# Kernel tuning notes

Hardware: AMD Instinct MI355X
Metric: run time of the kernel (lower is better)

The kernel has to match this reference:

```python
import jax, jax.numpy as jnp
import numpy as np

B, S, E, H = 2, 2048, 1024, 16
Dh = E // H
LN_EPS = 1e-5


def setup_inputs() -> dict:
    key = jax.random.key(0)
    ks = jax.random.split(key, 12)
    std = 1.0 / np.sqrt(E)
    inp = {
        "query": jax.random.normal(ks[0], (B, S, E), jnp.float32),
        "key":   jax.random.normal(ks[1], (B, S, E), jnp.float32),
        "value": jax.random.normal(ks[2], (B, S, E), jnp.float32),
        # True = masked. Causal mask so every row keeps >=1 valid entry.
        "mask": jnp.broadcast_to(jnp.triu(jnp.ones((S, S), bool), k=1), (B, S, S)),
        # per-head QKV projections, stacked: weight [H, Dh, E] (torch Linear layout), bias [H, Dh]
        "Wq_w": jax.random.uniform(ks[3], (H, Dh, E), jnp.float32, -std, std),
        "Wq_b": jax.random.uniform(ks[4], (H, Dh), jnp.float32, -std, std),
        "Wk_w": jax.random.uniform(ks[5], (H, Dh, E), jnp.float32, -std, std),
        "Wk_b": jax.random.uniform(ks[6], (H, Dh), jnp.float32, -std, std),
        "Wv_w": jax.random.uniform(ks[7], (H, Dh, E), jnp.float32, -std, std),
        "Wv_b": jax.random.uniform(ks[8], (H, Dh), jnp.float32, -std, std),
        # output projection [E, E] (torch layout: out = x @ W.T + b)
        "out_w": jax.random.uniform(ks[9], (E, E), jnp.float32, -std, std),
        "out_b": jax.random.uniform(ks[10], (E,), jnp.float32, -std, std),
        "ln_g": jnp.ones((E,), jnp.float32),
        "ln_b": jnp.zeros((E,), jnp.float32),
    }
    return inp


def reference(query, key, value, mask, Wq_w, Wq_b, Wk_w, Wk_b, Wv_w, Wv_b, out_w, out_b, ln_g, ln_b):
    # per-head projections (batched over heads): [B,S,E] x [H,Dh,E] -> [B,H,S,Dh]
    q = jnp.einsum('bse,hde->bhsd', query, Wq_w) + Wq_b[None, :, None, :]
    k = jnp.einsum('bse,hde->bhsd', key,   Wk_w) + Wk_b[None, :, None, :]
    v = jnp.einsum('bse,hde->bhsd', value, Wv_w) + Wv_b[None, :, None, :]
    scale = 1.0 / np.sqrt(Dh).astype(np.float32)
    scores = jnp.einsum('bhsd,bhtd->bhst', q, k) * scale  # [B,H,S,S]
    scores = jnp.where(mask[:, None, :, :], -jnp.inf, scores)
    probs = jax.nn.softmax(scores, axis=-1)  # dropout p=0 (eval)
    ctx = jnp.einsum('bhst,bhtd->bhsd', probs, v)  # [B,H,S,Dh]
    att = ctx.transpose(0, 2, 1, 3).reshape(query.shape[0], query.shape[1], -1)  # concat heads [B,S,E]
    proj = att @ out_w.T + out_b  # dropout p=0
    x = query + proj  # residual
    mu = jnp.mean(x, axis=-1, keepdims=True)
    var = jnp.mean(jnp.square(x - mu), axis=-1, keepdims=True)
    return (x - mu) * jax.lax.rsqrt(var + LN_EPS) * ln_g + ln_b
```

## Files before the change

kernel.cpp:

```cpp
#include <hip/hip_runtime.h>
#include <stdint.h>

#define B_ 2
#define S_ 2048
#define E_ 1024
#define H_ 16
#define DH 64
#define M_TOT (B_*S_)

typedef short s16x8 __attribute__((ext_vector_type(8)));
typedef float f32x4 __attribute__((ext_vector_type(4)));
typedef unsigned int u32;
typedef unsigned short u16;

union V8 { uint4 u; s16x8 v; };

__device__ __forceinline__ u32 fbits(float f){ union{float f;u32 i;}x; x.f=f; return x.i; }
__device__ __forceinline__ u32 prround(float f){ return fbits(f)+0x8000u; }
__device__ __forceinline__ u16 f2bf(float f){ return (u16)(prround(f)>>16); }
__device__ __forceinline__ u32 permpack(u32 hi,u32 lo){ return __builtin_amdgcn_perm(hi,lo,0x07060302u); }
__device__ __forceinline__ uint4 pack8r(const float4 a, const float4 b){
    uint4 p;
    p.x = permpack(prround(a.y),prround(a.x));
    p.y = permpack(prround(a.w),prround(a.z));
    p.z = permpack(prround(b.y),prround(b.x));
    p.w = permpack(prround(b.w),prround(b.z));
    return p;
}
__device__ __forceinline__ float exp2_fast(float x){ float r; asm("v_exp_f32 %0, %1":"=v"(r):"v"(x)); return r; }

typedef const __attribute__((address_space(1))) u32* gas_t;
typedef __attribute__((address_space(3))) u32* las_t;
#define GLDS16(gp, lp) __builtin_amdgcn_global_load_lds((gas_t)(gp), (las_t)(lp), 16, 0, 0)

__global__ __launch_bounds__(256) void cvtw(
    const float* __restrict__ w0, const float* __restrict__ w1, const float* __restrict__ w2,
    u16* __restrict__ dst, int n4)
{
    const int z = blockIdx.y;
    const float* s = (z==0)?w0:(z==1)?w1:w2;
    u16* d = dst + (size_t)z*E_*E_;
    int i = blockIdx.x*256 + threadIdx.x;
    const int stride = gridDim.x*256;
    for (; i<n4; i+=stride){
        float4 v = ((const float4*)s)[i];
        uint2 p;
        p.x = permpack(prround(v.y),prround(v.x));
        p.y = permpack(prround(v.w),prround(v.z));
        ((uint2*)d)[i] = p;
    }
}
__global__ __launch_bounds__(256) void cvt1(
    const float* __restrict__ s, u16* __restrict__ d, int n4)
{
    int i = blockIdx.x*256 + threadIdx.x;
    const int stride = gridDim.x*256;
    for (; i<n4; i+=stride){
        float4 v = ((const float4*)s)[i];
        uint2 p;
        p.x = permpack(prround(v.y),prround(v.x));
        p.y = permpack(prround(v.w),prround(v.z));
        ((uint2*)d)[i] = p;
    }
}

__global__ __launch_bounds__(256) void qkv128(
    const float* __restrict__ xq, const float* __restrict__ xk, const float* __restrict__ xv,
    const u16* __restrict__ Wb,
    const float* __restrict__ bq, const float* __restrict__ bk, const float* __restrict__ bv,
    u16* __restrict__ oq, u16* __restrict__ ok_, u16* __restrict__ ovt)
{
    const int bid = blockIdx.x;
    const int c = bid & 7;
    const int t = bid >> 3;
    const int n = t & 7;
    const int g = ((t >> 3) << 3) + c;
    const int m = g & 31, z = g >> 5;

    const float* X = (z==0)?xq:(z==1)?xk:xv;
    const u16* W = Wb + (size_t)z*E_*E_;
    const float* bia = (z==0)?bq:(z==1)?bk:bv;
    const float scale = (z==0)? 0.125f*1.44269504f : 1.0f;

    __shared__ __align__(16) float As0[128*32];
    __shared__ __align__(16) float As1[128*32];
    __shared__ __align__(16) u16  Bs0[128*32];
    __shared__ __align__(16) u16  Bs1[128*32];

    const int tid = threadIdx.x;
    const int wid = tid>>6, lane = tid&63;
    const int lrow = lane&15, quad = lane>>4;
    const int mb = m*128, nb = n*128;
    const int wm = (wid>>1)*64, wn = (wid&1)*64;
    const int arow = lane>>3, akq = lane&7;
    const int brow = lane>>2, bkq = lane&3;

    f32x4 acc[4][4] = {};
    const float* Xb = X + (size_t)mb*E_;
    const u16*  Wn = W + (size_t)nb*E_;

    auto stage = [&](float* Ad, u16* Bd, int k0){
#pragma unroll
        for (int i=0;i<4;i++){
            const int rb = wid*32 + i*8;
            GLDS16(Xb + (size_t)(rb+arow)*E_ + k0 + ((akq^arow)<<2), Ad + rb*32);
        }
#pragma unroll
        for (int i=0;i<2;i++){
            const int rb = wid*32 + i*16;
            GLDS16(Wn + (size_t)(rb+brow)*E_ + k0 + (bkq<<3), Bd + rb*32);
        }
    };
    auto compute = [&](const float* Ad, const u16* Bd){
        s16x8 af[4], bfr[4];
#pragma unroll
        for (int mi=0;mi<4;mi++){
            const int row = wm+mi*16+lrow;
            const int sw = lrow&7;
            const float4 fa = *(const float4*)&Ad[row*32 + (((quad<<1)   )^sw)*4];
            const float4 fb = *(const float4*)&Ad[row*32 + (((quad<<1)|1 )^sw)*4];
            V8 tt; tt.u = pack8r(fa, fb);
            af[mi] = tt.v;
        }
#pragma unroll
        for (int ci=0;ci<4;ci++)
            bfr[ci] = *(const s16x8*)&Bd[(wn+ci*16+lrow)*32 + quad*8];
#pragma unroll
        for (int mi=0;mi<4;mi++)
#pragma unroll
            for (int ci=0;ci<4;ci++)
                acc[mi][ci] = __builtin_amdgcn_mfma_f32_16x16x32_bf16(af[mi], bfr[ci], acc[mi][ci],0,0,0);
    };

    stage(As0, Bs0, 0);
    for (int k0=0; k0<E_; k0+=64){
        __syncthreads();
        if (k0+32 < E_) stage(As1, Bs1, k0+32);
        compute(As0, Bs0);
        __syncthreads();
        if (k0+64 < E_) stage(As0, Bs0, k0+64);
        compute(As1, Bs1);
    }

    if (z < 2){
        u16* O = (z==0)?oq:ok_;
#pragma unroll
        for (int ci=0;ci<4;ci++){
            const int nn = nb+wn+ci*16+lrow;
            const float bval = bia[nn];
            const int h = nn>>6, d = nn&63;
#pragma unroll
            for (int mi=0;mi<4;mi++){
#pragma unroll
                for (int r=0;r<4;r++){
                    const int mm = mb+wm+mi*16+quad*4+r;
                    const int bb = mm>>11, s = mm&(S_-1);
                    O[(((size_t)(bb*H_+h))*S_+s)*DH + d] = f2bf((acc[mi][ci][r]+bval)*scale);
                }
            }
        }
    } else {
#pragma unroll
        for (int ci=0;ci<4;ci++){
            const int nn = nb+wn+ci*16+lrow;
            const float bval = bia[nn];
            const int h = nn>>6, d = nn&63;
#pragma unroll
            for (int mi=0;mi<4;mi++){
                const int m0 = mb+wm+mi*16+quad*4;
                const int bb = m0>>11, s0 = m0&(S_-1);
                uint2 pk;
                pk.x = permpack(prround(acc[mi][ci][1]+bval), prround(acc[mi][ci][0]+bval));
                pk.y = permpack(prround(acc[mi][ci][3]+bval), prround(acc[mi][ci][2]+bval));
                *(uint2*)&ovt[(((size_t)(bb*H_+h))*DH + d)*S_ + s0] = pk;
            }
        }
    }
}

__global__ __launch_bounds__(256) void attn(
    const u16* __restrict__ q_ws, const u16* __restrict__ k_ws,
    const u16* __restrict__ vt_ws, u16* __restrict__ att)
{
    const int bid = blockIdx.x;
    const int c8 = bid & 7;
    const int t = bid >> 3;
    const int p = t & 15;
    const int bh = ((t >> 4) << 3) + c8;
    const int b = bh>>4, h = bh&15;

    const u16* Qb = q_ws + (size_t)bh*S_*DH;
    const u16* Kb = k_ws + (size_t)bh*S_*DH;
    const u16* VT = vt_ws + (size_t)bh*DH*S_;

    __shared__ __align__(16) u16 Ks0[64*64];
    __shared__ __align__(16) u16 Ks1[64*64];
    __shared__ __align__(16) u16 Vt0[64*64];
    __shared__ __align__(16) u16 Vt1[64*64];
    __shared__ __align__(16) u16 Ps[4][16*64];

    const int tid = threadIdx.x;
    const int wid = tid>>6, lane = tid&63;
    const int lrow = lane&15, quad = lane>>4;
    u16* Pw = Ps[wid];

    const int srw = lane>>3;
    const int scs = lane&7;
    const int sgc = scs ^ srw;

    auto stageKV = [&](u16* Kd, u16* Vd, int t0){
#pragma unroll
        for (int g2=0; g2<2; g2++){
            const int rg = wid*16 + g2*8 + srw;
            GLDS16(Kb + (size_t)(t0+rg)*DH + (sgc<<3), Kd + (wid*16+g2*8)*64);
            GLDS16(VT + (size_t)rg*S_ + t0 + (sgc<<3), Vd + (wid*16+g2*8)*64);
        }
    };

    for (int ph=0; ph<2; ph++){
        const int qi = ph ? (31-p) : p;
        const int qb = qi<<6;

        s16x8 qf[2];
#pragma unroll
        for (int ch=0;ch<2;ch++)
            qf[ch] = *(const s16x8*)&Qb[(size_t)(qb+wid*16+lrow)*DH + ch*32 + quad*8];

        f32x4 o[4] = {};
        float l_lane = 0.f;
        const int qglob = qb + wid*16 + lrow;
        const int ntile = qi + 1;

        auto computeTile = [&](const u16* Kd, const u16* Vd, int t0, bool diag){
            f32x4 st[4] = {};
#pragma unroll
            for (int tt=0;tt<4;tt++){
                const int tr = tt*16+lrow;
#pragma unroll
                for (int ch=0;ch<2;ch++){
                    const int slot = (ch*4+quad) ^ (lrow&7);
                    const s16x8 kf = *(const s16x8*)&Kd[tr*64 + slot*8];
                    st[tt] = __builtin_amdgcn_mfma_f32_16x16x32_bf16(kf, qf[ch], st[tt],0,0,0);
                }
            }
            if (diag){
#pragma unroll
                for (int tt=0;tt<4;tt++){
                    const int tg = t0 + tt*16 + quad*4;
#pragma unroll
                    for (int r=0;r<4;r++)
                        if (tg + r > qglob) st[tt][r] = -1e30f;
                }
            }
#pragma unroll
            for (int tt=0;tt<4;tt++){
                const float p0 = exp2_fast(st[tt][0]);
                const float p1 = exp2_fast(st[tt][1]);
                const float p2 = exp2_fast(st[tt][2]);
                const float p3 = exp2_fast(st[tt][3]);
                l_lane += (p0+p1)+(p2+p3);
                const int tc = tt*2 + (quad>>1);
                const int ts = tc ^ (lrow&7);
                const int a0 = lrow*64 + ts*8 + (quad&1)*4;
                *(u32*)&Pw[a0]   = permpack(prround(p1),prround(p0));
                *(u32*)&Pw[a0+2] = permpack(prround(p3),prround(p2));
            }
            s16x8 pb[2];
#pragma unroll
            for (int ch=0;ch<2;ch++){
                const int slot = (ch*4+quad) ^ (lrow&7);
                pb[ch] = *(const s16x8*)&Pw[lrow*64 + slot*8];
            }
#pragma unroll
            for (int cc=0;cc<4;cc++){
                const int vr = cc*16+lrow;
#pragma unroll
                for (int ch=0;ch<2;ch++){
                    const int slot = (ch*4+quad) ^ (lrow&7);
                    const s16x8 vf = *(const s16x8*)&Vd[vr*64 + slot*8];
                    o[cc] = __builtin_amdgcn_mfma_f32_16x16x32_bf16(vf, pb[ch], o[cc],0,0,0);
                }
            }
        };

        __syncthreads();
        stageKV(Ks0, Vt0, 0);
        for (int ti=0; ; ti+=2){
            __syncthreads();
            if (ti+1 < ntile) stageKV(Ks1, Vt1, (ti+1)<<6);
            computeTile(Ks0, Vt0, ti<<6, ti==ntile-1);
            if (ti+1 >= ntile) break;
            __syncthreads();
            if (ti+2 < ntile) stageKV(Ks0, Vt0, (ti+2)<<6);
            computeTile(Ks1, Vt1, (ti+1)<<6, ti+1==ntile-1);
            if (ti+2 >= ntile) break;
        }

        float s = l_lane;
        s += __shfl_xor(s, 16, 64);
        s += __shfl_xor(s, 32, 64);
        const float rl = 1.0f/s;

#pragma unroll
        for (int cc=0;cc<4;cc++){
            uint2 pk;
            pk.x = permpack(prround(o[cc][1]*rl), prround(o[cc][0]*rl));
            pk.y = permpack(prround(o[cc][3]*rl), prround(o[cc][2]*rl));
            *(uint2*)&att[(size_t)(b*S_ + qglob)*E_ + h*DH + cc*16 + quad*4] = pk;
        }
    }
}

__global__ __launch_bounds__(256) void oproj128(
    const u16* __restrict__ A, const u16* __restrict__ W, const float* __restrict__ bias,
    const float* __restrict__ resid, float* __restrict__ out)
{
    const int bid = blockIdx.x;
    const int c = bid & 7;
    const int t = bid >> 3;
    const int n = t & 15;
    const int m = ((t >> 4) << 3) + c;

    __shared__ __align__(16) u16 As0[128*32];
    __shared__ __align__(16) u16 As1[128*32];
    __shared__ __align__(16) u16 Bs0[64*32];
    __shared__ __align__(16) u16 Bs1[64*32];

    const int tid = threadIdx.x;
    const int wid = tid>>6, lane = tid&63;
    const int lrow = lane&15, quad = lane>>4;
    const int mb = m*128, nb = n*64;
    const int srow = lane>>2, skq = lane&3;

    f32x4 acc[2][4] = {};
    const u16* Ab = A + (size_t)mb*E_;
    const u16* Wn = W + (size_t)nb*E_;

    auto stage = [&](u16* Ad, u16* Bd, int k0){
#pragma unroll
        for (int i=0;i<2;i++){
            const int rb = wid*32 + i*16;
            GLDS16(Ab + (size_t)(rb+srow)*E_ + k0 + (skq<<3), Ad + rb*32);
        }
        GLDS16(Wn + (size_t)(wid*16+srow)*E_ + k0 + (skq<<3), Bd + (wid*16)*32);
    };
    auto compute = [&](const u16* Ad, const u16* Bd){
        s16x8 af[2], bfr[4];
#pragma unroll
        for (int mi=0;mi<2;mi++)
            af[mi] = *(const s16x8*)&Ad[(wid*32+mi*16+lrow)*32 + quad*8];
#pragma unroll
        for (int ci=0;ci<4;ci++)
            bfr[ci] = *(const s16x8*)&Bd[(ci*16+lrow)*32 + quad*8];
#pragma unroll
        for (int mi=0;mi<2;mi++)
#pragma unroll
            for (int ci=0;ci<4;ci++)
                acc[mi][ci] = __builtin_amdgcn_mfma_f32_16x16x32_bf16(af[mi], bfr[ci], acc[mi][ci],0,0,0);
    };

    stage(As0, Bs0, 0);
    for (int k0=0; k0<E_; k0+=64){
        __syncthreads();
        if (k0+32 < E_) stage(As1, Bs1, k0+32);
        compute(As0, Bs0);
        __syncthreads();
        if (k0+64 < E_) stage(As0, Bs0, k0+64);
        compute(As1, Bs1);
    }

#pragma unroll
    for (int ci=0;ci<4;ci++){
        const int nn = nb+ci*16+lrow;
        const float bval = bias[nn];
#pragma unroll
        for (int mi=0;mi<2;mi++){
#pragma unroll
            for (int r=0;r<4;r++){
                const int mm = mb+wid*32+mi*16+quad*4+r;
                out[(size_t)mm*E_+nn] = acc[mi][ci][r] + bval + resid[(size_t)mm*E_+nn];
            }
        }
    }
}

__global__ __launch_bounds__(256) void ln_k(
    const float* __restrict__ xin, const float* __restrict__ lg,
    const float* __restrict__ lb, float* __restrict__ out)
{
    const int row = blockIdx.x;
    const int tid = threadIdx.x;
    const int wid = tid>>6, lane = tid&63;
    const float* xr = xin + (size_t)row*E_;

    float x[4];
    float s = 0.f;
#pragma unroll
    for (int i=0;i<4;i++){ const int e = i*256+tid; x[i] = xr[e]; s += x[i]; }
    __shared__ float red[8];
#pragma unroll
    for (int off=32; off>0; off>>=1) s += __shfl_xor(s, off, 64);
    if (lane==0) red[wid] = s;
    __syncthreads();
    const float mu = (red[0]+red[1]+red[2]+red[3]) * (1.f/E_);

    float v = 0.f;
#pragma unroll
    for (int i=0;i<4;i++){ const float d = x[i]-mu; v += d*d; }
#pragma unroll
    for (int off=32; off>0; off>>=1) v += __shfl_xor(v, off, 64);
    if (lane==0) red[wid+4] = v;
    __syncthreads();
    const float var = (red[4]+red[5]+red[6]+red[7]) * (1.f/E_);
    const float rs = rsqrtf(var + 1e-5f);

#pragma unroll
    for (int i=0;i<4;i++){
        const int e = i*256+tid;
        out[(size_t)row*E_+e] = (x[i]-mu)*rs*lg[e] + lb[e];
    }
}

extern "C" void kernel_launch(void* const* d_in, const int* in_sizes, int n_in,
                              void* d_out, int out_size, void* d_ws, size_t ws_size,
                              hipStream_t stream) {
    const float* q_in = (const float*)d_in[0];
    const float* k_in = (const float*)d_in[1];
    const float* v_in = (const float*)d_in[2];
    const float* wq = (const float*)d_in[4];
    const float* bq = (const float*)d_in[5];
    const float* wk = (const float*)d_in[6];
    const float* bk = (const float*)d_in[7];
    const float* wv = (const float*)d_in[8];
    const float* bv = (const float*)d_in[9];
    const float* ow = (const float*)d_in[10];
    const float* ob = (const float*)d_in[11];
    const float* lg = (const float*)d_in[12];
    const float* lb = (const float*)d_in[13];
    float* out = (float*)d_out;

    char* ws = (char*)d_ws;
    const size_t MB = (size_t)1<<20;
    u16* q_ws  = (u16*)(ws);
    u16* k_ws  = (u16*)(ws +  8*MB);
    u16* vt_ws = (u16*)(ws + 16*MB);
    u16* att   = (u16*)(ws + 24*MB);
    u16* Wbf   = (u16*)(ws + 24*MB);
    u16* owbf  = (u16*)(ws + 16*MB);
    float* proj = (float*)ws;

    cvtw<<<dim3(512,3), 256, 0, stream>>>(wq, wk, wv, Wbf, (E_*E_)/4);
    qkv128<<<dim3(768), 256, 0, stream>>>(
        q_in, k_in, v_in, Wbf, bq, bk, bv, q_ws, k_ws, vt_ws);
    attn<<<dim3(512), 256, 0, stream>>>(q_ws, k_ws, vt_ws, att);
    cvt1<<<dim3(1024), 256, 0, stream>>>(ow, owbf, (E_*E_)/4);
    oproj128<<<dim3(512), 256, 0, stream>>>(att, owbf, ob, q_in, proj);
    ln_k<<<dim3(M_TOT), 256, 0, stream>>>(proj, lg, lb, out);
}
```

Before: 271.2 us.

## Convert QKV activations to bf16 in registers, triple-buffer shared memory, swizzle tiles

The QKV projection kernel now loads fp32 activations into registers, packs them to bf16 once, and stores them to shared memory in bf16. Before, fp32 tiles were staged in LDS and converted on every fragment read. LDS is now a 3-stage ring, so one barrier per k-step replaces two, and launch bounds request 3 blocks per CU. XOR swizzles on the B tiles in QKV and on both tiles in the output-projection kernel aim to cut LDS bank conflicts. The cost is more register pressure from holding the activation loads across the compute step, and the A loads now go through registers instead of direct-to-LDS loads.

Result: faster. 258.2 us (-4.8%).

```diff
diff --git a/kernel.cpp b/kernel.cpp
--- a/kernel.cpp
+++ b/kernel.cpp
@@ -64,7 +64,7 @@
     }
 }
 
-__global__ __launch_bounds__(256) void qkv128(
+__global__ __launch_bounds__(256,3) void qkv128(
     const float* __restrict__ xq, const float* __restrict__ xk, const float* __restrict__ xv,
     const u16* __restrict__ Wb,
     const float* __restrict__ bq, const float* __restrict__ bk, const float* __restrict__ bv,
@@ -82,49 +82,52 @@
     const float* bia = (z==0)?bq:(z==1)?bk:bv;
     const float scale = (z==0)? 0.125f*1.44269504f : 1.0f;
 
-    __shared__ __align__(16) float As0[128*32];
-    __shared__ __align__(16) float As1[128*32];
-    __shared__ __align__(16) u16  Bs0[128*32];
-    __shared__ __align__(16) u16  Bs1[128*32];
+    __shared__ __align__(16) u16 AsAll[3*128*32];
+    __shared__ __align__(16) u16 BsAll[3*128*32];
 
     const int tid = threadIdx.x;
     const int wid = tid>>6, lane = tid&63;
     const int lrow = lane&15, quad = lane>>4;
     const int mb = m*128, nb = n*128;
     const int wm = (wid>>1)*64, wn = (wid&1)*64;
-    const int arow = lane>>3, akq = lane&7;
-    const int brow = lane>>2, bkq = lane&3;
+    const int srow = lane>>2, skq = lane&3;
+    const int arow = wid*32 + (lane>>1);
+    const int akh  = lane&1;
 
     f32x4 acc[4][4] = {};
     const float* Xb = X + (size_t)mb*E_;
     const u16*  Wn = W + (size_t)nb*E_;
-
-    auto stage = [&](float* Ad, u16* Bd, int k0){
-#pragma unroll
-        for (int i=0;i<4;i++){
-            const int rb = wid*32 + i*8;
-            GLDS16(Xb + (size_t)(rb+arow)*E_ + k0 + ((akq^arow)<<2), Ad + rb*32);
-        }
+    const float* Xrow = Xb + (size_t)arow*E_ + akh*16;
+
+    float4 ar[4];
+    auto issueA = [&](int k0){
+#pragma unroll
+        for (int i=0;i<4;i++) ar[i] = *(const float4*)(Xrow + k0 + i*4);
+    };
+    auto writeA = [&](u16* Ad){
+        const int g0 = akh*2;
+        const int sw = arow&3;
+        const uint4 w0 = pack8r(ar[0], ar[1]);
+        const uint4 w1 = pack8r(ar[2], ar[3]);
+        *(uint4*)&Ad[arow*32 + ((g0  )^sw)*8] = w0;
+        *(uint4*)&Ad[arow*32 + ((g0+1)^sw)*8] = w1;
+    };
+    auto stageB = [&](u16* Bd, int k0){
 #pragma unroll
         for (int i=0;i<2;i++){
             const int rb = wid*32 + i*16;
-            GLDS16(Wn + (size_t)(rb+brow)*E_ + k0 + (bkq<<3), Bd + rb*32);
-        }
-    };
-    auto compute = [&](const float* Ad, const u16* Bd){
+            GLDS16(Wn + (size_t)(rb+srow)*E_ + k0 + ((skq^(srow&3))<<3), Bd + rb*32);
+        }
+    };
+    auto compute = [&](const u16* Ad, const u16* Bd){
         s16x8 af[4], bfr[4];
-#pragma unroll
-        for (int mi=0;mi<4;mi++){
-            const int row = wm+mi*16+lrow;
-            const int sw = lrow&7;
-            const float4 fa = *(const float4*)&Ad[row*32 + (((quad<<1)   )^sw)*4];
-            const float4 fb = *(const float4*)&Ad[row*32 + (((quad<<1)|1 )^sw)*4];
-            V8 tt; tt.u = pack8r(fa, fb);
-            af[mi] = tt.v;
-        }
+        const int sw = lrow&3;
+#pragma unroll
+        for (int mi=0;mi<4;mi++)
+            af[mi] = *(const s16x8*)&Ad[(wm+mi*16+lrow)*32 + (quad^sw)*8];
 #pragma unroll
         for (int ci=0;ci<4;ci++)
-            bfr[ci] = *(const s16x8*)&Bd[(wn+ci*16+lrow)*32 + quad*8];
+            bfr[ci] = *(const s16x8*)&Bd[(wn+ci*16+lrow)*32 + (quad^sw)*8];
 #pragma unroll
         for (int mi=0;mi<4;mi++)
 #pragma unroll
@@ -132,14 +135,25 @@
                 acc[mi][ci] = __builtin_amdgcn_mfma_f32_16x16x32_bf16(af[mi], bfr[ci], acc[mi][ci],0,0,0);
     };
 
-    stage(As0, Bs0, 0);
-    for (int k0=0; k0<E_; k0+=64){
+    issueA(0);
+    stageB(BsAll, 0);
+    writeA(AsAll);
+
+    int cur = 0, nxt = 1;
+    for (int it=0; it<32; ++it){
+        u16* Ac = AsAll + cur*(128*32);
+        u16* Bc = BsAll + cur*(128*32);
+        u16* An = AsAll + nxt*(128*32);
+        u16* Bn = BsAll + nxt*(128*32);
         __syncthreads();
-        if (k0+32 < E_) stage(As1, Bs1, k0+32);
-        compute(As0, Bs0);
-        __syncthreads();
-        if (k0+64 < E_) stage(As0, Bs0, k0+64);
-        compute(As1, Bs1);
+        if (it+1 < 32){
+            issueA((it+1)*32);
+            stageB(Bn, (it+1)*32);
+        }
+        compute(Ac, Bc);
+        if (it+1 < 32) writeA(An);
+        cur = nxt;
+        nxt = nxt+1; if (nxt==3) nxt=0;
     }
 
     if (z < 2){
@@ -337,21 +351,23 @@
     const u16* Wn = W + (size_t)nb*E_;
 
     auto stage = [&](u16* Ad, u16* Bd, int k0){
+        const int kc = (skq^(srow&3))<<3;
 #pragma unroll
         for (int i=0;i<2;i++){
             const int rb = wid*32 + i*16;
-            GLDS16(Ab + (size_t)(rb+srow)*E_ + k0 + (skq<<3), Ad + rb*32);
-        }
-        GLDS16(Wn + (size_t)(wid*16+srow)*E_ + k0 + (skq<<3), Bd + (wid*16)*32);
+            GLDS16(Ab + (size_t)(rb+srow)*E_ + k0 + kc, Ad + rb*32);
+        }
+        GLDS16(Wn + (size_t)(wid*16+srow)*E_ + k0 + kc, Bd + (wid*16)*32);
     };
     auto compute = [&](const u16* Ad, const u16* Bd){
         s16x8 af[2], bfr[4];
+        const int sw = lrow&3;
 #pragma unroll
         for (int mi=0;mi<2;mi++)
-            af[mi] = *(const s16x8*)&Ad[(wid*32+mi*16+lrow)*32 + quad*8];
+            af[mi] = *(const s16x8*)&Ad[(wid*32+mi*16+lrow)*32 + (quad^sw)*8];
 #pragma unroll
         for (int ci=0;ci<4;ci++)
-            bfr[ci] = *(const s16x8*)&Bd[(ci*16+lrow)*32 + quad*8];
+            bfr[ci] = *(const s16x8*)&Bd[(ci*16+lrow)*32 + (quad^sw)*8];
 #pragma unroll
         for (int mi=0;mi<2;mi++)
 #pragma unroll
```
